# Kernel optimization log

Hardware: AMD Instinct MI355X
Metric: run time of the kernel (lower is better)

## Reference

```python
import jax, jax.numpy as jnp
import numpy as np

N = 50000      # nodes
E = 800000     # edges (avg degree 16)
IN = 256       # in_dim == heads*hidden (so DGL residual is Identity)
H = 4          # heads
D = 64         # hidden_dim / out_dim per head
EPS = 1e-5
NEG_SLOPE_ATTN = 0.2   # DGL GATConv edge-attention leaky_relu slope
NEG_SLOPE_ACT = 0.01   # F.leaky_relu default


def gat_conv(x, src, dst, W, al, ar, b, act):
    # x: [N, H*D], W: [H*D, H*D], al/ar: [H, D], b: [H*D]
    feat = (x @ W).reshape(N, H, D)                       # [N,H,D]
    el = jnp.sum(feat * al, axis=-1)                      # [N,H]
    er = jnp.sum(feat * ar, axis=-1)                      # [N,H]
    e = jax.nn.leaky_relu(el[src] + er[dst], NEG_SLOPE_ATTN)  # [E,H]
    # segment softmax over incoming edges per destination node
    m = jax.ops.segment_max(e, dst, num_segments=N)       # [N,H]
    m = jnp.where(jnp.isfinite(m), m, 0.0)                # nodes with no in-edges
    ee = jnp.exp(e - m[dst])                              # [E,H]
    denom = jax.ops.segment_sum(ee, dst, num_segments=N)  # [N,H]
    alpha = ee / jnp.maximum(denom[dst], 1e-9)            # [E,H]
    msg = feat[src] * alpha[:, :, None]                   # [E,H,D]
    rst = jax.ops.segment_sum(msg, dst, num_segments=N)   # [N,H,D]
    rst = rst + x.reshape(N, H, D)                        # identity residual (dims match)
    rst = rst + b.reshape(1, H, D)
    if act:
        rst = jax.nn.leaky_relu(rst, NEG_SLOPE_ACT)
    return rst


def batch_norm(h, gamma, beta):
    # BatchNorm1d in training mode: batch statistics over node dim
    mu = jnp.mean(h, axis=0)
    var = jnp.var(h, axis=0)
    return (h - mu) * jax.lax.rsqrt(var + EPS) * gamma + beta


def setup_inputs():
    key = jax.random.key(0)
    ks = jax.random.split(key, 18)
    s = 1.0 / np.sqrt(IN)
    inp = {
        'x': jax.random.normal(ks[0], (N, IN), jnp.float32),
        'src': jax.random.randint(ks[1], (E,), 0, N),
        'dst': jax.random.randint(ks[2], (E,), 0, N),
    }
    names = ['W1', 'al1', 'ar1', 'b1', 'W2', 'al2', 'ar2', 'b2', 'W3', 'al3', 'ar3', 'b3']
    shapes = [(IN, H * D), (H, D), (H, D), (H * D,)] * 3
    for i, (nm, sh) in enumerate(zip(names, shapes)):
        inp[nm] = jax.random.normal(ks[3 + i], sh, jnp.float32) * s
    inp['g1'] = jnp.ones((H * D,), jnp.float32)
    inp['be1'] = jnp.zeros((H * D,), jnp.float32)
    inp['g2'] = jnp.ones((H * D,), jnp.float32)
    inp['be2'] = jnp.zeros((H * D,), jnp.float32)
    return inp


def reference(x, src, dst, W1, al1, ar1, b1, W2, al2, ar2, b2, W3, al3, ar3, b3, g1, be1, g2, be2):
    h = gat_conv(x, src, dst, W1, al1, ar1, b1, act=True).reshape(N, H * D)
    h = batch_norm(h, g1, be1)
    h = gat_conv(h, src, dst, W2, al2, ar2, b2, act=True).reshape(N, H * D)
    h = batch_norm(h, g2, be2)
    h = gat_conv(h, src, dst, W3, al3, ar3, b3, act=False)   # [N,H,D]
    return h.mean(axis=1)                                    # [N,D]
```

## Files before the change

kernel.cpp:

```cpp
#include <hip/hip_runtime.h>

constexpr int NN = 50000;
constexpr int NE = 800000;
constexpr float SLOPE_A = 0.2f;
constexpr float SLOPE_R = 0.01f;
constexpr int SCB = 196;

typedef __attribute__((ext_vector_type(8))) short bf16x8;
typedef __attribute__((ext_vector_type(4))) float f32x4;

__device__ __forceinline__ unsigned short f2bf(float f) {
    union { float f; unsigned u; } v; v.f = f;
    unsigned u = v.u;
    unsigned r = u + 0x7fffu + ((u >> 16) & 1u);
    return (unsigned short)(r >> 16);
}
__device__ __forceinline__ float bf2f(unsigned short s) {
    union { unsigned u; float f; } v; v.u = ((unsigned)s) << 16;
    return v.f;
}
__device__ __forceinline__ float bflo(unsigned u) {
    union { unsigned u; float f; } v; v.u = u << 16; return v.f;
}
__device__ __forceinline__ float bfhi(unsigned u) {
    union { unsigned u; float f; } v; v.u = u & 0xffff0000u; return v.f;
}

__global__ void k_hist(const int* __restrict__ dst, int* __restrict__ cnt) {
    int i = blockIdx.x * 256 + threadIdx.x;
    if (i < NE) atomicAdd(&cnt[dst[i]], 1);
}

__global__ void k_scan1(const int* __restrict__ cnt, int* __restrict__ loc,
                        int* __restrict__ bsum) {
    __shared__ int sh[256];
    int t = threadIdx.x;
    int i = blockIdx.x * 256 + t;
    int v = (i < NN) ? cnt[i] : 0;
    sh[t] = v;
    __syncthreads();
    for (int off = 1; off < 256; off <<= 1) {
        int tmp = (t >= off) ? sh[t - off] : 0;
        __syncthreads();
        sh[t] += tmp;
        __syncthreads();
    }
    loc[i] = sh[t] - v;
    if (t == 255) bsum[blockIdx.x] = sh[255];
}

__global__ void k_scan2(const int* __restrict__ bsum, int* __restrict__ boff,
                        int* __restrict__ rowptr) {
    __shared__ int sh[256];
    int t = threadIdx.x;
    int v = (t < SCB) ? bsum[t] : 0;
    sh[t] = v;
    __syncthreads();
    for (int off = 1; off < 256; off <<= 1) {
        int tmp = (t >= off) ? sh[t - off] : 0;
        __syncthreads();
        sh[t] += tmp;
        __syncthreads();
    }
    if (t < SCB) boff[t] = sh[t] - v;
    if (t == 255) rowptr[NN] = sh[255];
}

__global__ void k_scan3(const int* __restrict__ loc, const int* __restrict__ boff,
                        int* __restrict__ rowptr, int* __restrict__ cursor) {
    int i = blockIdx.x * 256 + threadIdx.x;
    if (i < NN) {
        int r = loc[i] + boff[blockIdx.x];
        rowptr[i] = r;
        cursor[i] = r;
    }
}

__global__ void k_scatter(const int* __restrict__ src, const int* __restrict__ dst,
                          int* __restrict__ cursor, int* __restrict__ ssrc,
                          int* __restrict__ sdst) {
    int i = blockIdx.x * 256 + threadIdx.x;
    if (i < NE) {
        int d = dst[i];
        int pos = atomicAdd(&cursor[d], 1);
        ssrc[pos] = src[i];
        sdst[pos] = d;
    }
}

__global__ void k_fold(const float* __restrict__ W, const float* __restrict__ sc,
                       const float* __restrict__ sh, const float* __restrict__ al,
                       const float* __restrict__ ar, unsigned short* __restrict__ Wfrag,
                       float* __restrict__ cvec, unsigned short* __restrict__ wlrfrag,
                       float* __restrict__ offlr, int has_bn) {
    int b = blockIdx.x;
    if (b < 32) {
        int gid = b * 256 + threadIdx.x;
        int lane = gid & 63;
        int frag = gid >> 6;
        int j = frag & 3, kc = (frag >> 2) & 7, w = frag >> 5;
        int mm = lane & 15, q = lane >> 4;
        int n = 64 * w + 16 * j + mm;
        int k0 = kc * 32 + q * 8;
        unsigned short o[8];
#pragma unroll
        for (int t = 0; t < 8; t++) {
            float wv = W[(size_t)(k0 + t) * 256 + n];
            if (sc) wv *= sc[k0 + t];
            o[t] = f2bf(wv);
        }
        *(uint4*)(Wfrag + (size_t)gid * 8) = *(const uint4*)o;
    } else if (has_bn && b < 288) {
        __shared__ float red[256];
        int n = b - 32, k = threadIdx.x;
        red[k] = sh[k] * W[(size_t)k * 256 + n];
        __syncthreads();
        for (int off = 128; off > 0; off >>= 1) {
            if (k < off) red[k] += red[k + off];
            __syncthreads();
        }
        if (k == 0) cvec[n] = red[0];
    } else {
        int n = b - (has_bn ? 288 : 32);
        int h = n >> 1;
        const float* a = (n & 1) ? ar : al;
        int k = threadIdx.x;
        float raw = 0.f;
#pragma unroll 8
        for (int d = 0; d < 64; d++)
            raw += W[(size_t)k * 256 + 64 * h + d] * a[h * 64 + d];
        float val = (sc ? sc[k] : 1.f) * raw;
        int kc = k >> 5, rem = k & 31, q = rem >> 3, t = rem & 7;
        wlrfrag[kc * 512 + (q * 16 + n) * 8 + t] = f2bf(val);
        wlrfrag[kc * 512 + (q * 16 + n + 8) * 8 + t] = 0;
        __shared__ float red[256];
        red[k] = sh ? sh[k] * raw : 0.f;
        __syncthreads();
        for (int off = 128; off > 0; off >>= 1) {
            if (k < off) red[k] += red[k + off];
            __syncthreads();
        }
        if (k == 0) offlr[n] = red[0];
    }
}

__launch_bounds__(256)
__global__ void k_gemm(const void* __restrict__ Araw, int af32,
                       const unsigned short* __restrict__ Wfrag,
                       const float* __restrict__ cvec,
                       const unsigned short* __restrict__ wlrfrag,
                       const float* __restrict__ offlr,
                       unsigned short* __restrict__ feat16, float* __restrict__ el,
                       float* __restrict__ er) {
    constexpr int AP = 264;
    __shared__ __align__(16) unsigned short Alds[64 * AP];
    const int tid = threadIdx.x;
    const int rowbase = blockIdx.x * 64;

    if (af32) {
        const float* A = (const float*)Araw;
        int r = tid >> 6;
        int c4 = tid & 63;
        for (int it = 0; it < 16; it++) {
            int rr = it * 4 + r;
            int gr = rowbase + rr;
            float4 v = make_float4(0.f, 0.f, 0.f, 0.f);
            if (gr < NN) v = *(const float4*)(A + (size_t)gr * 256 + c4 * 4);
            ushort4 pv;
            pv.x = f2bf(v.x); pv.y = f2bf(v.y); pv.z = f2bf(v.z); pv.w = f2bf(v.w);
            *(ushort4*)(&Alds[rr * AP + c4 * 4]) = pv;
        }
    } else {
        const unsigned short* A = (const unsigned short*)Araw;
        for (int it = 0; it < 8; it++) {
            int idx = it * 256 + tid;
            int rr = idx >> 5;
            int c16 = idx & 31;
            int gr = rowbase + rr;
            uint4 v = make_uint4(0u, 0u, 0u, 0u);
            if (gr < NN) v = *(const uint4*)(A + (size_t)gr * 256 + c16 * 8);
            *(uint4*)(&Alds[rr * AP + c16 * 8]) = v;
        }
    }
    __syncthreads();

    f32x4 acc[4][4];
    for (int i = 0; i < 4; i++)
        for (int j = 0; j < 4; j++)
            acc[i][j] = (f32x4){0.f, 0.f, 0.f, 0.f};
    f32x4 accLR[4];
    for (int i = 0; i < 4; i++) accLR[i] = (f32x4){0.f, 0.f, 0.f, 0.f};

    const int lane = tid & 63, w = tid >> 6;
    const int mm = lane & 15, q = lane >> 4;

    const unsigned short* bbase = Wfrag + ((size_t)w * 8 * 4) * 512 + (size_t)lane * 8;

#pragma unroll
    for (int kc = 0; kc < 8; kc++) {
        bf16x8 a[4], b[4];
        for (int i = 0; i < 4; i++)
            a[i] = *(const bf16x8*)(&Alds[(16 * i + mm) * AP + kc * 32 + q * 8]);
        for (int j = 0; j < 4; j++)
            b[j] = *(const bf16x8*)(bbase + (size_t)(kc * 4 + j) * 512);
        for (int i = 0; i < 4; i++)
            for (int j = 0; j < 4; j++)
                acc[i][j] = __builtin_amdgcn_mfma_f32_16x16x32_bf16(a[i], b[j], acc[i][j], 0, 0, 0);
        if (w == 0) {
            bf16x8 blr = *(const bf16x8*)(wlrfrag + kc * 512 + lane * 8);
            for (int i = 0; i < 4; i++)
                accLR[i] = __builtin_amdgcn_mfma_f32_16x16x32_bf16(a[i], blr, accLR[i], 0, 0, 0);
        }
    }
    __syncthreads();

    if (cvec) {
        float cv[4];
        for (int j = 0; j < 4; j++) cv[j] = cvec[64 * w + 16 * j + mm];
        for (int i = 0; i < 4; i++)
            for (int j = 0; j < 4; j++)
                for (int r = 0; r < 4; r++)
                    acc[i][j][r] += cv[j];
    }

    if (w == 0 && mm < 8) {
        float off = offlr[mm];
        int h = mm >> 1;
        float* dstp = (mm & 1) ? er : el;
        for (int i = 0; i < 4; i++)
            for (int r = 0; r < 4; r++) {
                int gr = rowbase + 16 * i + q * 4 + r;
                if (gr < NN) dstp[gr * 4 + h] = accLR[i][r] + off;
            }
    }

    for (int i = 0; i < 4; i++)
        for (int j = 0; j < 4; j++) {
            int gc = 64 * w + 16 * j + mm;
            for (int r = 0; r < 4; r++) {
                int rr = 16 * i + q * 4 + r;
                Alds[rr * AP + gc] = f2bf(acc[i][j][r]);
            }
        }
    __syncthreads();
    for (int it = 0; it < 8; it++) {
        int idx = it * 256 + tid;
        int rr = idx >> 5;
        int c16 = idx & 31;
        int gr = rowbase + rr;
        if (gr < NN)
            *(uint4*)(feat16 + (size_t)gr * 256 + c16 * 8) = *(const uint4*)(&Alds[rr * AP + c16 * 8]);
    }
}

__global__ void k_wgt(const int* __restrict__ ssrc, const int* __restrict__ sdst,
                      const float* __restrict__ el, const float* __restrict__ er,
                      float* __restrict__ wgt) {
    int pos = blockIdx.x * 256 + threadIdx.x;
    if (pos >= NE) return;
    int s = ssrc[pos], dd = sdst[pos];
    float4 a = *(const float4*)(el + (size_t)s * 4);
    float4 b = *(const float4*)(er + (size_t)dd * 4);
    float4 o;
    float v;
    v = a.x + b.x; v = (v > 0.f) ? v : SLOPE_A * v; o.x = __expf(v);
    v = a.y + b.y; v = (v > 0.f) ? v : SLOPE_A * v; o.y = __expf(v);
    v = a.z + b.z; v = (v > 0.f) ? v : SLOPE_A * v; o.z = __expf(v);
    v = a.w + b.w; v = (v > 0.f) ? v : SLOPE_A * v; o.w = __expf(v);
    *(float4*)(wgt + (size_t)pos * 4) = o;
}

__launch_bounds__(256)
__global__ void k_agg(const unsigned short* __restrict__ feat16,
                      const float* __restrict__ wgt,
                      const int* __restrict__ rowptr, const int* __restrict__ ssrc,
                      const unsigned short* __restrict__ residh, const float* __restrict__ residf,
                      const float* __restrict__ bnscale, const float* __restrict__ bnshift,
                      int use_bn, const float* __restrict__ bias, int act,
                      unsigned short* __restrict__ outh, float* __restrict__ outf,
                      int final_mean) {
    int n = __builtin_amdgcn_readfirstlane(blockIdx.x * 4 + (threadIdx.x >> 6));
    int l = threadIdx.x & 63;
    int p = l >> 5;
    int q = l & 31;
    int c8 = q * 8;
    int hh = q >> 3;
    int beg = rowptr[n], end = rowptr[n + 1];

    float r[8];
    if (residf) {
        float4 r0 = *(const float4*)(residf + (size_t)n * 256 + c8);
        float4 r1 = *(const float4*)(residf + (size_t)n * 256 + c8 + 4);
        r[0] = r0.x; r[1] = r0.y; r[2] = r0.z; r[3] = r0.w;
        r[4] = r1.x; r[5] = r1.y; r[6] = r1.z; r[7] = r1.w;
    } else {
        uint4 rv = *(const uint4*)(residh + (size_t)n * 256 + c8);
        r[0] = bflo(rv.x); r[1] = bfhi(rv.x);
        r[2] = bflo(rv.y); r[3] = bfhi(rv.y);
        r[4] = bflo(rv.z); r[5] = bfhi(rv.z);
        r[6] = bflo(rv.w); r[7] = bfhi(rv.w);
    }

    float d = 0.f;
    float acc[8];
#pragma unroll
    for (int k = 0; k < 8; k++) acc[k] = 0.f;

    for (int e = beg; e < end; e += 8) {
        int ss[4];
        float ww[4];
        uint4 ff[4];
#pragma unroll
        for (int s = 0; s < 4; s++) {
            int idx = e + 2 * s + p;
            int cidx = (idx < end) ? idx : beg;
            ss[s] = ssrc[cidx];
            float wv = wgt[(size_t)cidx * 4 + hh];
            ww[s] = (idx < end) ? wv : 0.f;
        }
#pragma unroll
        for (int s = 0; s < 4; s++)
            ff[s] = *(const uint4*)(feat16 + (size_t)ss[s] * 256 + c8);
#pragma unroll
        for (int s = 0; s < 4; s++) {
            float w = ww[s];
            d += w;
            acc[0] += bflo(ff[s].x) * w; acc[1] += bfhi(ff[s].x) * w;
            acc[2] += bflo(ff[s].y) * w; acc[3] += bfhi(ff[s].y) * w;
            acc[4] += bflo(ff[s].z) * w; acc[5] += bfhi(ff[s].z) * w;
            acc[6] += bflo(ff[s].w) * w; acc[7] += bfhi(ff[s].w) * w;
        }
    }

    d += __shfl_xor(d, 32, 64);
#pragma unroll
    for (int k = 0; k < 8; k++) acc[k] += __shfl_xor(acc[k], 32, 64);

    float invd = 1.f / fmaxf(d, 1e-9f);
#pragma unroll
    for (int k = 0; k < 8; k++) acc[k] *= invd;

    if (use_bn) {
        float4 s0 = *(const float4*)(bnscale + c8);
        float4 s1 = *(const float4*)(bnscale + c8 + 4);
        float4 h0 = *(const float4*)(bnshift + c8);
        float4 h1 = *(const float4*)(bnshift + c8 + 4);
        r[0] = r[0] * s0.x + h0.x; r[1] = r[1] * s0.y + h0.y;
        r[2] = r[2] * s0.z + h0.z; r[3] = r[3] * s0.w + h0.w;
        r[4] = r[4] * s1.x + h1.x; r[5] = r[5] * s1.y + h1.y;
        r[6] = r[6] * s1.z + h1.z; r[7] = r[7] * s1.w + h1.w;
    }
    {
        float4 b0 = *(const float4*)(bias + c8);
        float4 b1 = *(const float4*)(bias + c8 + 4);
        acc[0] += r[0] + b0.x; acc[1] += r[1] + b0.y;
        acc[2] += r[2] + b0.z; acc[3] += r[3] + b0.w;
        acc[4] += r[4] + b1.x; acc[5] += r[5] + b1.y;
        acc[6] += r[6] + b1.z; acc[7] += r[7] + b1.w;
    }
    if (act) {
#pragma unroll
        for (int k = 0; k < 8; k++) acc[k] = (acc[k] > 0.f) ? acc[k] : SLOPE_R * acc[k];
    }

    if (!final_mean) {
        if (p == 0) {
            uint4 o;
            o.x = (unsigned)f2bf(acc[0]) | ((unsigned)f2bf(acc[1]) << 16);
            o.y = (unsigned)f2bf(acc[2]) | ((unsigned)f2bf(acc[3]) << 16);
            o.z = (unsigned)f2bf(acc[4]) | ((unsigned)f2bf(acc[5]) << 16);
            o.w = (unsigned)f2bf(acc[6]) | ((unsigned)f2bf(acc[7]) << 16);
            *(uint4*)(outh + (size_t)n * 256 + c8) = o;
        }
    } else {
#pragma unroll
        for (int k = 0; k < 8; k++) {
            acc[k] += __shfl_xor(acc[k], 8, 64);
            acc[k] += __shfl_xor(acc[k], 16, 64);
        }
        if (p == 0 && q < 8) {
            float4 o0 = make_float4(acc[0] * 0.25f, acc[1] * 0.25f, acc[2] * 0.25f, acc[3] * 0.25f);
            float4 o1 = make_float4(acc[4] * 0.25f, acc[5] * 0.25f, acc[6] * 0.25f, acc[7] * 0.25f);
            *(float4*)(outf + (size_t)n * 64 + c8) = o0;
            *(float4*)(outf + (size_t)n * 64 + c8 + 4) = o1;
        }
    }
}

__global__ void k_bnstats(const unsigned short* __restrict__ hh, float* __restrict__ pbuf) {
    __shared__ float ps[8 * 256];
    __shared__ float ps2[8 * 256];
    int t = threadIdx.x, b = blockIdx.x;
    int r8 = t >> 5, c32 = t & 31;
    int r0 = b * 196, r1 = min(r0 + 196, NN);
    float s[8], s2[8];
#pragma unroll
    for (int e = 0; e < 8; e++) { s[e] = 0.f; s2[e] = 0.f; }
    for (int r = r0 + r8; r < r1; r += 8) {
        uint4 v = *(const uint4*)(hh + (size_t)r * 256 + c32 * 8);
        const unsigned short* pv = (const unsigned short*)&v;
#pragma unroll
        for (int e = 0; e < 8; e++) {
            float f = bf2f(pv[e]);
            s[e] += f; s2[e] += f * f;
        }
    }
#pragma unroll
    for (int e = 0; e < 8; e++) {
        ps[r8 * 256 + c32 * 8 + e] = s[e];
        ps2[r8 * 256 + c32 * 8 + e] = s2[e];
    }
    __syncthreads();
    float ts = 0.f, ts2 = 0.f;
    for (int g = 0; g < 8; g++) { ts += ps[g * 256 + t]; ts2 += ps2[g * 256 + t]; }
    pbuf[b * 512 + t] = ts;
    pbuf[b * 512 + 256 + t] = ts2;
}

__global__ void k_bnfinal(const float* __restrict__ pbuf, const float* __restrict__ g,
                          const float* __restrict__ be, float* __restrict__ scale,
                          float* __restrict__ shift) {
    int t = threadIdx.x;
    float s = 0.f, s2 = 0.f;
    for (int b = 0; b < 256; b++) {
        s += pbuf[b * 512 + t];
        s2 += pbuf[b * 512 + 256 + t];
    }
    float mu = s * (1.f / NN);
    float var = s2 * (1.f / NN) - mu * mu;
    float rs = rsqrtf(var + 1e-5f);
    float sc = rs * g[t];
    scale[t] = sc;
    shift[t] = be[t] - mu * sc;
}

extern "C" void kernel_launch(void* const* d_in, const int* in_sizes, int n_in,
                              void* d_out, int out_size, void* d_ws, size_t ws_size,
                              hipStream_t stream) {
    const float* x   = (const float*)d_in[0];
    const int* src   = (const int*)d_in[1];
    const int* dst   = (const int*)d_in[2];
    const float* W1  = (const float*)d_in[3];
    const float* al1 = (const float*)d_in[4];
    const float* ar1 = (const float*)d_in[5];
    const float* b1  = (const float*)d_in[6];
    const float* W2  = (const float*)d_in[7];
    const float* al2 = (const float*)d_in[8];
    const float* ar2 = (const float*)d_in[9];
    const float* b2  = (const float*)d_in[10];
    const float* W3  = (const float*)d_in[11];
    const float* al3 = (const float*)d_in[12];
    const float* ar3 = (const float*)d_in[13];
    const float* b3  = (const float*)d_in[14];
    const float* g1  = (const float*)d_in[15];
    const float* be1 = (const float*)d_in[16];
    const float* g2  = (const float*)d_in[17];
    const float* be2 = (const float*)d_in[18];
    float* out = (float*)d_out;

    char* ws = (char*)d_ws;
    size_t off = 0;
    auto alloc = [&](size_t bytes) {
        void* p = ws + off;
        off += (bytes + 255) & ~(size_t)255;
        return p;
    };
    int* rowptr = (int*)alloc((NN + 1) * sizeof(int));
    int* cursor = (int*)alloc(NN * sizeof(int));
    int* cnt    = (int*)alloc(SCB * 256 * sizeof(int));
    int* loc    = (int*)alloc(SCB * 256 * sizeof(int));
    int* bsum   = (int*)alloc(SCB * sizeof(int));
    int* boff   = (int*)alloc(SCB * sizeof(int));
    int* ssrc   = (int*)alloc(NE * sizeof(int));
    int* sdst   = (int*)alloc(NE * sizeof(int));
    float* wgt  = (float*)alloc((size_t)NE * 4 * sizeof(float));
    unsigned short* feat16 = (unsigned short*)alloc((size_t)NN * 256 * sizeof(unsigned short));
    unsigned short* hbuf   = (unsigned short*)alloc((size_t)NN * 256 * sizeof(unsigned short));
    float* el   = (float*)alloc((size_t)NN * 4 * sizeof(float));
    float* er   = (float*)alloc((size_t)NN * 4 * sizeof(float));
    unsigned short* Wfrag1  = (unsigned short*)alloc(65536 * sizeof(unsigned short));
    unsigned short* Wfrag2  = (unsigned short*)alloc(65536 * sizeof(unsigned short));
    unsigned short* wlrfrag = (unsigned short*)alloc(4096 * sizeof(unsigned short));
    float* offlr   = (float*)alloc(16 * sizeof(float));
    float* cvec    = (float*)alloc(256 * sizeof(float));
    float* pbuf    = (float*)alloc(256 * 512 * sizeof(float));
    float* bnscale = (float*)alloc(256 * sizeof(float));
    float* bnshift = (float*)alloc(256 * sizeof(float));

    hipMemsetAsync(cnt, 0, NN * sizeof(int), stream);
    k_hist<<<(NE + 255) / 256, 256, 0, stream>>>(dst, cnt);
    k_scan1<<<SCB, 256, 0, stream>>>(cnt, loc, bsum);
    k_scan2<<<1, 256, 0, stream>>>(bsum, boff, rowptr);
    k_scan3<<<SCB, 256, 0, stream>>>(loc, boff, rowptr, cursor);
    k_scatter<<<(NE + 255) / 256, 256, 0, stream>>>(src, dst, cursor, ssrc, sdst);
    k_fold<<<40, 256, 0, stream>>>(W1, nullptr, nullptr, al1, ar1,
                                   Wfrag1, nullptr, wlrfrag, offlr, 0);

    const int GB = (NN + 63) / 64;
    const int NB = NN / 4;
    const int EB = (NE + 255) / 256;

    k_gemm<<<GB, 256, 0, stream>>>(x, 1, Wfrag1, nullptr, wlrfrag, offlr, feat16, el, er);
    k_wgt<<<EB, 256, 0, stream>>>(ssrc, sdst, el, er, wgt);
    k_agg<<<NB, 256, 0, stream>>>(feat16, wgt, rowptr, ssrc, nullptr, x,
                                  nullptr, nullptr, 0, b1, 1, hbuf, nullptr, 0);
    k_bnstats<<<256, 256, 0, stream>>>(hbuf, pbuf);
    k_bnfinal<<<1, 256, 0, stream>>>(pbuf, g1, be1, bnscale, bnshift);
    k_fold<<<296, 256, 0, stream>>>(W2, bnscale, bnshift, al2, ar2,
                                    Wfrag2, cvec, wlrfrag, offlr, 1);

    k_gemm<<<GB, 256, 0, stream>>>(hbuf, 0, Wfrag2, cvec, wlrfrag, offlr, feat16, el, er);
    k_wgt<<<EB, 256, 0, stream>>>(ssrc, sdst, el, er, wgt);
    k_agg<<<NB, 256, 0, stream>>>(feat16, wgt, rowptr, ssrc, hbuf, nullptr,
                                  bnscale, bnshift, 1, b2, 1, hbuf, nullptr, 0);
    k_bnstats<<<256, 256, 0, stream>>>(hbuf, pbuf);
    k_bnfinal<<<1, 256, 0, stream>>>(pbuf, g2, be2, bnscale, bnshift);
    k_fold<<<296, 256, 0, stream>>>(W3, bnscale, bnshift, al3, ar3,
                                    Wfrag2, cvec, wlrfrag, offlr, 1);

    k_gemm<<<GB, 256, 0, stream>>>(hbuf, 0, Wfrag2, cvec, wlrfrag, offlr, feat16, el, er);
    k_wgt<<<EB, 256, 0, stream>>>(ssrc, sdst, el, er, wgt);
    k_agg<<<NB, 256, 0, stream>>>(feat16, wgt, rowptr, ssrc, hbuf, nullptr,
                                  bnscale, bnshift, 1, b3, 0, nullptr, out, 1);
}
```

Measured before the change: 558.7 us.

## Fuse edge-weight computation into aggregation kernel and drop sdst/wgt buffers

Removes the separate k_wgt pass and computes the leaky-relu/exp attention weight per edge inside k_agg. Each lane handles one (edge, head) pair for 16 edges, then weights and source ids are broadcast with wave shuffles. This also widens the aggregation batch from 8 to 16 edges per iteration. It eliminates writing and re-reading a 12.8MB weight buffer plus the sdst array each layer, at the cost of extra shuffles and register pressure inside the aggregation loop.

After: 565.2 us. Within noise of the previous version (+1.1%).

```diff
diff --git a/kernel.cpp b/kernel.cpp
--- a/kernel.cpp
+++ b/kernel.cpp
@@ -77,14 +77,12 @@
 }
 
 __global__ void k_scatter(const int* __restrict__ src, const int* __restrict__ dst,
-                          int* __restrict__ cursor, int* __restrict__ ssrc,
-                          int* __restrict__ sdst) {
+                          int* __restrict__ cursor, int* __restrict__ ssrc) {
     int i = blockIdx.x * 256 + threadIdx.x;
     if (i < NE) {
         int d = dst[i];
         int pos = atomicAdd(&cursor[d], 1);
         ssrc[pos] = src[i];
-        sdst[pos] = d;
     }
 }
 
@@ -253,26 +251,9 @@
     }
 }
 
-__global__ void k_wgt(const int* __restrict__ ssrc, const int* __restrict__ sdst,
-                      const float* __restrict__ el, const float* __restrict__ er,
-                      float* __restrict__ wgt) {
-    int pos = blockIdx.x * 256 + threadIdx.x;
-    if (pos >= NE) return;
-    int s = ssrc[pos], dd = sdst[pos];
-    float4 a = *(const float4*)(el + (size_t)s * 4);
-    float4 b = *(const float4*)(er + (size_t)dd * 4);
-    float4 o;
-    float v;
-    v = a.x + b.x; v = (v > 0.f) ? v : SLOPE_A * v; o.x = __expf(v);
-    v = a.y + b.y; v = (v > 0.f) ? v : SLOPE_A * v; o.y = __expf(v);
-    v = a.z + b.z; v = (v > 0.f) ? v : SLOPE_A * v; o.z = __expf(v);
-    v = a.w + b.w; v = (v > 0.f) ? v : SLOPE_A * v; o.w = __expf(v);
-    *(float4*)(wgt + (size_t)pos * 4) = o;
-}
-
 __launch_bounds__(256)
 __global__ void k_agg(const unsigned short* __restrict__ feat16,
-                      const float* __restrict__ wgt,
+                      const float* __restrict__ el, const float* __restrict__ er,
                       const int* __restrict__ rowptr, const int* __restrict__ ssrc,
                       const unsigned short* __restrict__ residh, const float* __restrict__ residf,
                       const float* __restrict__ bnscale, const float* __restrict__ bnshift,
@@ -285,7 +266,10 @@
     int q = l & 31;
     int c8 = q * 8;
     int hh = q >> 3;
+    int wh = l & 3;
+    int we = l >> 2;
     int beg = rowptr[n], end = rowptr[n + 1];
+    float er_w = er[n * 4 + wh];
 
     float r[8];
     if (residf) {
@@ -306,23 +290,31 @@
 #pragma unroll
     for (int k = 0; k < 8; k++) acc[k] = 0.f;
 
-    for (int e = beg; e < end; e += 8) {
-        int ss[4];
-        float ww[4];
-        uint4 ff[4];
-#pragma unroll
-        for (int s = 0; s < 4; s++) {
-            int idx = e + 2 * s + p;
-            int cidx = (idx < end) ? idx : beg;
-            ss[s] = ssrc[cidx];
-            float wv = wgt[(size_t)cidx * 4 + hh];
-            ww[s] = (idx < end) ? wv : 0.f;
-        }
-#pragma unroll
-        for (int s = 0; s < 4; s++)
-            ff[s] = *(const uint4*)(feat16 + (size_t)ss[s] * 256 + c8);
-#pragma unroll
-        for (int s = 0; s < 4; s++) {
+    for (int e = beg; e < end; e += 16) {
+        int idx = e + we;
+        bool vld = idx < end;
+        int cidx = vld ? idx : beg;
+        int sw = ssrc[cidx];
+        float a = el[sw * 4 + wh];
+        float sc = a + er_w;
+        sc = (sc > 0.f) ? sc : SLOPE_A * sc;
+        float wl = vld ? __expf(sc) : 0.f;
+
+        int sn[8];
+        float ww[8];
+#pragma unroll
+        for (int s = 0; s < 8; s++) {
+            int eo = 2 * s + p;
+            sn[s] = __shfl(sw, eo * 4, 64);
+            ww[s] = __shfl(wl, eo * 4 + hh, 64);
+        }
+
+        uint4 ff[8];
+#pragma unroll
+        for (int s = 0; s < 8; s++)
+            ff[s] = *(const uint4*)(feat16 + (size_t)sn[s] * 256 + c8);
+#pragma unroll
+        for (int s = 0; s < 8; s++) {
             float w = ww[s];
             d += w;
             acc[0] += bflo(ff[s].x) * w; acc[1] += bfhi(ff[s].x) * w;
@@ -472,8 +464,6 @@
     int* bsum   = (int*)alloc(SCB * sizeof(int));
     int* boff   = (int*)alloc(SCB * sizeof(int));
     int* ssrc   = (int*)alloc(NE * sizeof(int));
-    int* sdst   = (int*)alloc(NE * sizeof(int));
-    float* wgt  = (float*)alloc((size_t)NE * 4 * sizeof(float));
     unsigned short* feat16 = (unsigned short*)alloc((size_t)NN * 256 * sizeof(unsigned short));
     unsigned short* hbuf   = (unsigned short*)alloc((size_t)NN * 256 * sizeof(unsigned short));
     float* el   = (float*)alloc((size_t)NN * 4 * sizeof(float));
@@ -492,17 +482,15 @@
     k_scan1<<<SCB, 256, 0, stream>>>(cnt, loc, bsum);
     k_scan2<<<1, 256, 0, stream>>>(bsum, boff, rowptr);
     k_scan3<<<SCB, 256, 0, stream>>>(loc, boff, rowptr, cursor);
-    k_scatter<<<(NE + 255) / 256, 256, 0, stream>>>(src, dst, cursor, ssrc, sdst);
+    k_scatter<<<(NE + 255) / 256, 256, 0, stream>>>(src, dst, cursor, ssrc);
     k_fold<<<40, 256, 0, stream>>>(W1, nullptr, nullptr, al1, ar1,
                                    Wfrag1, nullptr, wlrfrag, offlr, 0);
 
     const int GB = (NN + 63) / 64;
     const int NB = NN / 4;
-    const int EB = (NE + 255) / 256;
 
     k_gemm<<<GB, 256, 0, stream>>>(x, 1, Wfrag1, nullptr, wlrfrag, offlr, feat16, el, er);
-    k_wgt<<<EB, 256, 0, stream>>>(ssrc, sdst, el, er, wgt);
-    k_agg<<<NB, 256, 0, stream>>>(feat16, wgt, rowptr, ssrc, nullptr, x,
+    k_agg<<<NB, 256, 0, stream>>>(feat16, el, er, rowptr, ssrc, nullptr, x,
                                   nullptr, nullptr, 0, b1, 1, hbuf, nullptr, 0);
     k_bnstats<<<256, 256, 0, stream>>>(hbuf, pbuf);
     k_bnfinal<<<1, 256, 0, stream>>>(pbuf, g1, be1, bnscale, bnshift);
@@ -510,8 +498,7 @@
                                     Wfrag2, cvec, wlrfrag, offlr, 1);
 
     k_gemm<<<GB, 256, 0, stream>>>(hbuf, 0, Wfrag2, cvec, wlrfrag, offlr, feat16, el, er);
-    k_wgt<<<EB, 256, 0, stream>>>(ssrc, sdst, el, er, wgt);
-    k_agg<<<NB, 256, 0, stream>>>(feat16, wgt, rowptr, ssrc, hbuf, nullptr,
+    k_agg<<<NB, 256, 0, stream>>>(feat16, el, er, rowptr, ssrc, hbuf, nullptr,
                                   bnscale, bnshift, 1, b2, 1, hbuf, nullptr, 0);
     k_bnstats<<<256, 256, 0, stream>>>(hbuf, pbuf);
     k_bnfinal<<<1, 256, 0, stream>>>(pbuf, g2, be2, bnscale, bnshift);
@@ -519,7 +506,6 @@
                                     Wfrag2, cvec, wlrfrag, offlr, 1);
 
     k_gemm<<<GB, 256, 0, stream>>>(hbuf, 0, Wfrag2, cvec, wlrfrag, offlr, feat16, el, er);
-    k_wgt<<<EB, 256, 0, stream>>>(ssrc, sdst, el, er, wgt);
-    k_agg<<<NB, 256, 0, stream>>>(feat16, wgt, rowptr, ssrc, hbuf, nullptr,
+    k_agg<<<NB, 256, 0, stream>>>(feat16, el, er, rowptr, ssrc, hbuf, nullptr,
                                   bnscale, bnshift, 1, b3, 0, nullptr, out, 1);
 }
```
